# Performance work log

Measured on AMD Instinct MI355X. Metric: run time of the kernel, lower is better.

The kernel has to match this reference:

```python
import jax, jax.numpy as jnp
import numpy as np

NEG_INF = float('-inf')


def setup_inputs() -> dict:
    key = jax.random.key(0)
    ks = jax.random.split(key, 5)
    Sq, Sk, H, D, B = 4096, 4096, 8, 128, 4
    q = jax.random.normal(ks[0], (Sq, H, D), jnp.float32)
    k_local = jax.random.normal(ks[1], (Sk, H, D), jnp.float32)
    v_local = jax.random.normal(ks[2], (Sk, H, D), jnp.float32)
    k_remote = jax.random.normal(ks[3], (Sk, H, D), jnp.float32)
    v_remote = jax.random.normal(ks[4], (Sk, H, D), jnp.float32)
    # 4 ragged range pairs: equal blocks of 1024 q-tokens <-> 1024 kv-tokens
    blk = Sq // B
    starts = jnp.arange(B, dtype=jnp.int32) * blk
    ranges = jnp.stack([starts, starts + blk], axis=1)  # [B, 2]
    return dict(
        q=q, k_local=k_local, v_local=v_local,
        k_remote=k_remote, v_remote=v_remote,
        q_ranges_local=ranges, kv_ranges_local=ranges,
        is_causal_local=jnp.ones((B,), bool),
        q_ranges_remote=ranges, kv_ranges_remote=ranges,
        is_causal_remote=jnp.zeros((B,), bool),
    )


def _range_mask(Sq, Sk, q_ranges, kv_ranges, is_causal):
    # Build [Sq, Sk] attend-mask from ragged (q,kv) range pairs.
    qpos = jnp.arange(Sq)[None, :, None]   # [1, Sq, 1]
    kpos = jnp.arange(Sk)[None, None, :]   # [1, 1, Sk]
    qs = q_ranges[:, 0][:, None, None]; qe = q_ranges[:, 1][:, None, None]
    ks = kv_ranges[:, 0][:, None, None]; ke = kv_ranges[:, 1][:, None, None]
    in_q = (qpos >= qs) & (qpos < qe)
    in_k = (kpos >= ks) & (kpos < ke)
    # bottom-right-aligned causal within each range pair
    shift = (ke - ks) - (qe - qs)
    caus = (kpos - ks) <= (qpos - qs) + shift
    m = in_q & in_k & (caus | ~is_causal[:, None, None])  # [B, Sq, Sk]
    return jnp.any(m, axis=0)  # [Sq, Sk]


def _flex_attn(q, k, v, q_ranges, kv_ranges, is_causal):
    # q: [Sq, H, D]; k, v: [Sk, H, D] -> out [Sq, H, D], lse [H, Sq]
    Sq, H, D = q.shape
    Sk = k.shape[0]
    mask = _range_mask(Sq, Sk, q_ranges, kv_ranges, is_causal)  # [Sq, Sk]
    scale = 1.0 / np.sqrt(D).astype(np.float32)
    scores = jnp.einsum('qhd,khd->hqk', q, k) * scale
    scores = jnp.where(mask[None], scores, NEG_INF)
    mx = jnp.max(scores, axis=-1)                      # [H, Sq]
    mx_safe = jnp.where(jnp.isneginf(mx), 0.0, mx)
    e = jnp.where(mask[None], jnp.exp(scores - mx_safe[..., None]), 0.0)
    s = jnp.sum(e, axis=-1)                            # [H, Sq]
    lse = jnp.where(s > 0, mx_safe + jnp.log(jnp.where(s > 0, s, 1.0)), NEG_INF)
    p = e / jnp.where(s > 0, s, 1.0)[..., None]
    out = jnp.einsum('hqk,khd->qhd', p, v)
    return out, lse


def _safe_subtract(a, b):
    both_ninf = (a == b) & jnp.isneginf(a)
    return jnp.where(both_ninf, NEG_INF, a - b)


def _correct_lse(lse1, lse2):
    mn = jnp.minimum(lse1, lse2).astype(jnp.float32)
    mx = jnp.maximum(lse1, lse2).astype(jnp.float32)
    return (mx + jax.nn.softplus(_safe_subtract(mn, mx))).astype(lse1.dtype)


def _correct_out(o1, lse1, o2, lse2, lse):
    # lse*: [H, Sq] -> weights [Sq, H, 1]
    w1 = jnp.exp(_safe_subtract(lse1, lse)).T[..., None].astype(jnp.float32)
    w2 = jnp.exp(_safe_subtract(lse2, lse)).T[..., None].astype(jnp.float32)
    return (w1 * o1 + w2 * o2).astype(o1.dtype)


def _result_correction(out_list, lse_list, overlap_degree):
    # Faithful to the original loop structure (stage 1 merged twice).
    curr_lse = _correct_lse(lse_list[0], lse_list[1])
    curr_out = _correct_out(out_list[0], lse_list[0], out_list[1], lse_list[1], curr_lse)
    for i in range(overlap_degree):
        orig_lse, orig_out = curr_lse, curr_out
        curr_lse = _correct_lse(orig_lse, lse_list[i + 1])
        curr_out = _correct_out(orig_out, orig_lse, out_list[i + 1], lse_list[i + 1], curr_lse)
    return curr_out, curr_lse


def reference(q, k_local, v_local, k_remote, v_remote,
              q_ranges_local, kv_ranges_local, is_causal_local,
              q_ranges_remote, kv_ranges_remote, is_causal_remote):
    o0, l0 = _flex_attn(q, k_local, v_local, q_ranges_local, kv_ranges_local, is_causal_local)
    o1, l1 = _flex_attn(q, k_remote, v_remote, q_ranges_remote, kv_ranges_remote, is_causal_remote)
    out, lse = _result_correction([o0, o1], [l0, l1], overlap_degree=1)
    return out, lse
```

## Files before the change

kernel.cpp:

```cpp
#include <hip/hip_runtime.h>
#include <math.h>
#include <limits.h>


constexpr int NH = 8;
constexpr int DH = 128;
#define NEG_INF (-INFINITY)

typedef __bf16 bf16x8 __attribute__((ext_vector_type(8)));
typedef float  f32x4  __attribute__((ext_vector_type(4)));
typedef float  f32x16 __attribute__((ext_vector_type(16)));

__device__ __forceinline__ unsigned short f2bf_rne(float x) {
  union { float f; unsigned u; } v; v.f = x;
  unsigned r = v.u + 0x7FFFu + ((v.u >> 16) & 1u);
  return (unsigned short)(r >> 16);
}
__device__ __forceinline__ unsigned pk2(float lo, float hi) {
  return (unsigned)f2bf_rne(lo) | ((unsigned)f2bf_rne(hi) << 16);
}
__device__ __forceinline__ unsigned cvtpk_bf16(float lo, float hi) {
  unsigned r;
  asm("v_cvt_pk_bf16_f32 %0, %1, %2" : "=v"(r) : "v"(lo), "v"(hi));
  return r;
}
__device__ __forceinline__ void gl2lds16(const void* g, void* l) {
  __builtin_amdgcn_global_load_lds(
      (const __attribute__((address_space(1))) unsigned int*)g,
      (__attribute__((address_space(3))) unsigned int*)l, 16, 0, 0);
}
#define MFMA32 __builtin_amdgcn_mfma_f32_32x32x16_bf16

__global__ void prep_kernel(const float* __restrict__ kl, const float* __restrict__ kr,
                            const float* __restrict__ vl, const float* __restrict__ vr,
                            unsigned short* __restrict__ Kb,
                            unsigned short* __restrict__ Vt, int Sk) {
  __shared__ unsigned short T[64 * 132];
  const int nk = Sk >> 2;
  const int npan = Sk >> 6;
  const int t = threadIdx.x;
  int bid = blockIdx.x;

  if (bid < 2 * nk) {
    const int src = bid >= nk;
    const int x = src ? bid - nk : bid;
    const float* in = src ? kr : kl;
    unsigned short* o = Kb + (size_t)src * NH * Sk * DH;
    const size_t base = (size_t)x * 4096;
    #pragma unroll
    for (int rdx = 0; rdx < 4; ++rdx) {
      const size_t L = base + rdx * 1024 + (size_t)t * 4;
      float4 f = *(const float4*)(in + L);
      const int kv  = (int)(L >> 10);
      const int rem = (int)(L & 1023);
      const int h = rem >> 7, d = rem & 127;
      const int pe = (((d >> 3) ^ (kv & 7)) << 3) + (d & 7);
      uint2 w = make_uint2(pk2(f.x, f.y), pk2(f.z, f.w));
      *(uint2*)&o[((size_t)h * Sk + kv) * DH + pe] = w;
    }
  } else {
    bid -= 2 * nk;
    const int nv = npan * NH;
    const int src = bid >= nv;
    if (src) bid -= nv;
    const int h = bid / npan;
    const int x = bid % npan;
    const float* in = src ? vr : vl;
    const int kv0 = x * 64;
    unsigned short* panel =
        Vt + (((size_t)src * NH + h) * npan + x) * (DH * 64);
    {
      const int off = (t & 31) * 4;
      const int kvr_ = t >> 5;
      #pragma unroll
      for (int rdx = 0; rdx < 8; ++rdx) {
        const int kv = rdx * 8 + kvr_;
        float4 f = *(const float4*)(in + ((size_t)(kv0 + kv) * NH + h) * DH + off);
        *(uint2*)&T[kv * 132 + off] = make_uint2(pk2(f.x, f.y), pk2(f.z, f.w));
      }
    }
    __syncthreads();
    #pragma unroll
    for (int rdx = 0; rdx < 4; ++rdx) {
      const int G = rdx * 256 + t;
      const int d = G >> 3, gphys = G & 7;
      const int gk = gphys ^ (d & 7);
      unsigned short v[8];
      #pragma unroll
      for (int j = 0; j < 8; ++j) v[j] = T[(gk * 8 + j) * 132 + d];
      *(uint4*)&panel[(size_t)G * 8] = *(uint4*)v;
    }
  }
}

struct TS { int src, b, kv0, qs, qe, ks, ke, causal, shift, kendb; };

__global__ __launch_bounds__(256, 2)
void fa_kernel(const float* __restrict__ qp,
               const unsigned short* __restrict__ Kb,
               const unsigned short* __restrict__ Vt,
               const int* __restrict__ qrl, const int* __restrict__ kvrl,
               const int* __restrict__ czl,
               const int* __restrict__ qrr, const int* __restrict__ kvrr,
               const int* __restrict__ czr,
               float* __restrict__ outp, float* __restrict__ lsep,
               unsigned short* __restrict__ pO, float* __restrict__ pL,
               int Sq, int Sk, int B, int nsplit, int direct)
{
  __shared__ __align__(16) unsigned short Klds[2][64 * DH];
  __shared__ __align__(16) unsigned short Vlds[2][DH * 64];
  __shared__ float Lsc[4][32];

  const int tid = threadIdx.x, wave = tid >> 6, lane = tid & 63;
  const int dl = lane & 31, hi = lane >> 5;
  const int bid = blockIdx.x;
  const int h   = bid & 7;
  const int nqt = Sq >> 7;
  const int tt  = bid >> 3;
  int qtile = tt % nqt;
  const int split = tt / nqt;
  if (split & 1) qtile = nqt - 1 - qtile;
  const int q0 = qtile * 128;
  const int qw = q0 + wave * 32;
  const int qg = qw + dl;

  const float kscale = 0.12751743f;

  bf16x8 qfB[8];
  {
    const float* gq = qp + ((size_t)qg * NH + h) * DH + hi * 8;
    #pragma unroll
    for (int dc = 0; dc < 8; ++dc) {
      float4 a = *(const float4*)(gq + dc * 16);
      float4 b = *(const float4*)(gq + dc * 16 + 4);
      uint4 t = { pk2(a.x,a.y), pk2(a.z,a.w), pk2(b.x,b.y), pk2(b.z,b.w) };
      qfB[dc] = __builtin_bit_cast(bf16x8, t);
    }
  }

  f32x16 accO[4];
  #pragma unroll
  for (int i = 0; i < 4; ++i) accO[i] = (f32x16)(0.0f);
  float lacc = 0.0f;

  auto nextTile = [&](TS& t) -> bool {
    t.kv0 += nsplit * 64;
    while (t.kv0 >= t.kendb) {
      ++t.b;
      if (t.b >= B) {
        t.b = -1; ++t.src;
        if (t.src >= 2) return false;
        t.kendb = INT_MIN; t.kv0 = 0;
        continue;
      }
      const int* qr  = t.src ? qrr : qrl;
      const int* kvr = t.src ? kvrr : kvrl;
      const int* cz  = t.src ? czr : czl;
      t.qs = qr[2*t.b]; t.qe = qr[2*t.b+1];
      t.ks = kvr[2*t.b]; t.ke = kvr[2*t.b+1];
      if (t.qe <= q0 || t.qs >= q0 + 128 || t.ks >= t.ke) {
        t.kendb = INT_MIN; t.kv0 = 0; continue;
      }
      t.causal = cz[t.b] != 0;
      t.shift = (t.ke - t.ks) - (t.qe - t.qs);
      const int qmaxb = min(q0 + 127, t.qe - 1);
      t.kendb = t.causal ? min(t.ke, t.ks + (qmaxb - t.qs) + t.shift + 1) : t.ke;
      t.kv0 = ((t.ks >> 6) << 6) + split * 64;
    }
    return true;
  };

  auto stageTile = [&](const TS& t, int bi) {
    const unsigned short* kbh = Kb + ((size_t)t.src * NH + h) * (size_t)Sk * DH;
    const char* gk = (const char*)(kbh + (size_t)t.kv0 * DH) + wave * 4096 + lane * 16;
    char* lk = (char*)&Klds[bi][0] + wave * 4096 + lane * 16;
    #pragma unroll
    for (int i = 0; i < 4; ++i) gl2lds16(gk + i * 1024, lk + i * 1024);
    const unsigned short* vth = Vt + ((size_t)t.src * NH + h) * ((size_t)(Sk >> 6) * DH * 64);
    const char* gv = (const char*)(vth + (size_t)(t.kv0 >> 6) * (DH * 64)) + wave * 4096 + lane * 16;
    char* lv = (char*)&Vlds[bi][0] + wave * 4096 + lane * 16;
    #pragma unroll
    for (int i = 0; i < 4; ++i) gl2lds16(gv + i * 1024, lv + i * 1024);
  };

  TS cur; cur.src = 0; cur.b = -1; cur.kv0 = 0; cur.kendb = INT_MIN;
  cur.qs = 0; cur.qe = 0; cur.ks = 0; cur.ke = 0; cur.causal = 0; cur.shift = 0;
  bool haveCur = nextTile(cur);
  if (haveCur) stageTile(cur, 0);
  __syncthreads();
  int buf = 0;

  while (haveCur) {
    TS nxt = cur;
    const bool haveNxt = nextTile(nxt);
    if (haveNxt) stageTile(nxt, buf ^ 1);

    int wkend = INT_MIN;
    {
      const int wqs = max(qw, cur.qs), wqe = min(qw + 32, cur.qe);
      if (wqs < wqe) {
        const int wqmax = min(qw + 31, cur.qe - 1);
        wkend = cur.causal
              ? min(cur.ke, cur.ks + (wqmax - cur.qs) + cur.shift + 1)
              : cur.ke;
      }
    }

    if (cur.kv0 < wkend) {
      const int kv0 = cur.kv0, ks = cur.ks, ke = cur.ke;
      const int qs = cur.qs, qe = cur.qe, causal = cur.causal, shift = cur.shift;
      const float sbias = cur.src ? 1.0f : 0.0f;

      f32x16 S0 = (f32x16)(0.0f), S1 = (f32x16)(0.0f);
      const unsigned short* kb = &Klds[buf][0];
      __builtin_amdgcn_s_setprio(1);
      #pragma unroll
      for (int dc = 0; dc < 8; ++dc) {
        const int ph = ((dc * 2 + hi) ^ (dl & 7)) << 3;
        bf16x8 k0 = *(const bf16x8*)&kb[dl * DH + ph];
        bf16x8 k1 = *(const bf16x8*)&kb[(32 + dl) * DH + ph];
        S0 = MFMA32(k0, qfB[dc], S0, 0, 0, 0);
        S1 = MFMA32(k1, qfB[dc], S1, 0, 0, 0);
      }
      __builtin_amdgcn_s_setprio(0);

      const bool interior = (kv0 >= ks) && (kv0 + 64 <= ke) &&
                            (qw >= qs) && (qw + 32 <= qe) &&
                            (!causal || (kv0 + 63 - ks) <= (qw - qs) + shift);
      if (!interior) {
        const int qok = (qg >= qs) && (qg < qe);
        const int lo = ks - kv0;
        int up = ke - kv0 - 1;
        if (causal) up = min(up, (qg - qs) + shift + (ks - kv0));
        #pragma unroll
        for (int r = 0; r < 16; ++r) {
          const int kt = (r & 3) + 8 * (r >> 2) + 4 * hi;
          const int ok0 = qok && (kt >= lo) && (kt <= up);
          const int ok1 = qok && (kt + 32 >= lo) && (kt + 32 <= up);
          S0[r] = ok0 ? S0[r] : NEG_INF;
          S1[r] = ok1 ? S1[r] : NEG_INF;
        }
      }

      float p0[16], p1[16];
      #pragma unroll
      for (int r = 0; r < 16; ++r) {
        p0[r] = __builtin_amdgcn_exp2f(S0[r] * kscale + sbias);
        p1[r] = __builtin_amdgcn_exp2f(S1[r] * kscale + sbias);
      }
      {
        float t0 = 0.f, t1 = 0.f, t2 = 0.f, t3 = 0.f;
        #pragma unroll
        for (int r = 0; r < 4; ++r) {
          t0 += p0[r];      t1 += p0[r + 4];
          t2 += p0[r + 8];  t3 += p0[r + 12];
          t0 += p1[r];      t1 += p1[r + 4];
          t2 += p1[r + 8];  t3 += p1[r + 12];
        }
        lacc += (t0 + t1) + (t2 + t3);
      }

      __builtin_amdgcn_s_setprio(1);
      #define PVKC(pp, kc)                                                        \
      {                                                                           \
        const unsigned a0 = cvtpk_bf16(pp[((kc)&1)*8+0], pp[((kc)&1)*8+1]);       \
        const unsigned a1 = cvtpk_bf16(pp[((kc)&1)*8+2], pp[((kc)&1)*8+3]);       \
        const unsigned b0 = cvtpk_bf16(pp[((kc)&1)*8+4], pp[((kc)&1)*8+5]);       \
        const unsigned b1 = cvtpk_bf16(pp[((kc)&1)*8+6], pp[((kc)&1)*8+7]);       \
        auto s0 = __builtin_amdgcn_permlane32_swap((int)a0, (int)b0, false, false);\
        auto s1 = __builtin_amdgcn_permlane32_swap((int)a1, (int)b1, false, false);\
        uint4 pw = { (unsigned)s0[0], (unsigned)s1[0],                            \
                     (unsigned)s0[1], (unsigned)s1[1] };                          \
        const bf16x8 pa = __builtin_bit_cast(bf16x8, pw);                         \
        const int ph = (((kc) * 2 + hi) ^ (dl & 7)) << 3;                         \
        _Pragma("unroll")                                                         \
        for (int dt = 0; dt < 4; ++dt) {                                          \
          bf16x8 vf = *(const bf16x8*)&Vlds[buf][(dt * 32 + dl) * 64 + ph];       \
          accO[dt] = MFMA32(pa, vf, accO[dt], 0, 0, 0);                           \
        }                                                                         \
      }
      PVKC(p0, 0) PVKC(p0, 1) PVKC(p1, 2) PVKC(p1, 3)
      #undef PVKC
      __builtin_amdgcn_s_setprio(0);
    }

    __syncthreads();
    cur = nxt; haveCur = haveNxt; buf ^= 1;
  }

  const float tot = lacc + __shfl_xor(lacc, 32);
  if (lane < 32) Lsc[wave][lane] = tot;
  __syncthreads();

  if (direct) {
    if (lane < 32)
      lsep[(size_t)h * Sq + qg] =
          tot > 0.f ? 0.6931471805599453f * __builtin_amdgcn_logf(tot) : NEG_INF;
    #pragma unroll
    for (int r = 0; r < 16; ++r) {
      const int qrow = (r & 3) + 8 * (r >> 2) + 4 * hi;
      const float sum = Lsc[wave][qrow];
      const float rcp = sum > 0.f ? 1.0f / sum : 0.0f;
      float* op = outp + ((size_t)(qw + qrow) * NH + h) * DH + dl;
      #pragma unroll
      for (int dt = 0; dt < 4; ++dt)
        op[dt * 32] = accO[dt][r] * rcp;
    }
  } else {
    if (lane < 32) pL[((size_t)split * NH + h) * Sq + qg] = tot;
    #pragma unroll
    for (int r = 0; r < 16; ++r) {
      const int qrow = (r & 3) + 8 * (r >> 2) + 4 * hi;
      unsigned short* pr = pO + (((size_t)split * Sq + (qw + qrow)) * NH + h) * DH + dl;
      #pragma unroll
      for (int dt = 0; dt < 4; ++dt)
        pr[dt * 32] = f2bf_rne(accO[dt][r]);
    }
  }
}

__global__ void merge_kernel(const unsigned short* __restrict__ pO,
                             const float* __restrict__ pL,
                             float* __restrict__ outp, float* __restrict__ lsep,
                             int Sq, int nsplit) {
  const int t = threadIdx.x;
  const int row = blockIdx.x * 4 + (t >> 6);
  const int dp = t & 63;
  const int q = row >> 3, h = row & 7;
  float s = 0.f, o0 = 0.f, o1 = 0.f;
  for (int sp = 0; sp < nsplit; ++sp) {
    s += pL[((size_t)sp * NH + h) * Sq + q];
    unsigned u = *(const unsigned*)&pO[(((size_t)sp * Sq + q) * NH + h) * DH + dp * 2];
    o0 += __builtin_bit_cast(float, u << 16);
    o1 += __builtin_bit_cast(float, u & 0xffff0000u);
  }
  const float rcp = s > 0.f ? 1.0f / s : 0.f;
  *(float2*)&outp[(size_t)row * DH + dp * 2] = make_float2(o0 * rcp, o1 * rcp);
  if (dp == 0)
    lsep[(size_t)h * Sq + q] =
        s > 0.f ? 0.6931471805599453f * __builtin_amdgcn_logf(s) : NEG_INF;
}

extern "C" void kernel_launch(void* const* d_in, const int* in_sizes, int n_in,
                              void* d_out, int out_size, void* d_ws, size_t ws_size,
                              hipStream_t stream) {
  const float* qp = (const float*)d_in[0];
  const float* kl = (const float*)d_in[1];
  const float* vl = (const float*)d_in[2];
  const float* kr = (const float*)d_in[3];
  const float* vr = (const float*)d_in[4];
  const int* qrl  = (const int*)d_in[5];
  const int* kvrl = (const int*)d_in[6];
  const int* czl  = (const int*)d_in[7];
  const int* qrr  = (const int*)d_in[8];
  const int* kvrr = (const int*)d_in[9];
  const int* czr  = (const int*)d_in[10];

  const int B  = in_sizes[5] / 2;
  const int Sq = in_sizes[0] / (NH * DH);
  const int Sk = in_sizes[1] / (NH * DH);
  float* outp = (float*)d_out;
  float* lsep = outp + (size_t)Sq * NH * DH;

  const size_t TEN  = (size_t)NH * Sk * DH;
  const size_t base = 4 * TEN * sizeof(unsigned short);
  unsigned short* Kb = (unsigned short*)d_ws;
  unsigned short* Vt = Kb + 2 * TEN;

  auto needO = [&](int ns) {
    return (size_t)ns * Sq * NH * DH * 2 + (size_t)ns * NH * Sq * 4;
  };
  int ns; int direct = 0;
  if      (ws_size >= base + needO(2)) ns = 2;
  else if (ws_size >= base + needO(1)) ns = 1;
  else { ns = 1; direct = 1; }
  unsigned short* pO = (unsigned short*)((char*)d_ws + base);
  float* pL = (float*)((char*)d_ws + base + (size_t)ns * Sq * NH * DH * 2);

  const int prep_blocks = 2 * (Sk / 4) + 2 * (Sk / 64) * NH;
  prep_kernel<<<dim3(prep_blocks), 256, 0, stream>>>(kl, kr, vl, vr, Kb, Vt, Sk);

  fa_kernel<<<dim3(ns * (Sq / 128) * NH), 256, 0, stream>>>(
      qp, Kb, Vt, qrl, kvrl, czl, qrr, kvrr, czr,
      outp, lsep, pO, pL, Sq, Sk, B, ns, direct);

  if (!direct)
    merge_kernel<<<dim3(Sq * NH / 4), 256, 0, stream>>>(pO, pL, outp, lsep, Sq, ns);
}
```

Measured before the change: 178.2 us.

## Rework K/V LDS swizzles, fold softmax scale into Q, unroll double-buffer loop

Widens the K swizzle from 8 to 16 chunks and changes the V panel layout so two d-rows share each 128-element row with an XOR swizzle, aiming to cut LDS bank conflicts. The softmax scale moves into the Q bf16 conversion and the remote-source factor of two moves into V preprocessing and the row-sum accumulation, which removes a per-element FMA before exp2. The main loop is manually unrolled by two so buffer indices are compile-time constants. Pre-scaling Q before the bf16 rounding changes rounding behaviour slightly, and the unbalanced-tile shortcut in the unrolled loop needs care to stay correct.

Measured after the change: 177.2 us. About the same (-0.6%).

```diff
diff --git a/kernel.cpp b/kernel.cpp
--- a/kernel.cpp
+++ b/kernel.cpp
@@ -54,7 +54,7 @@
       const int kv  = (int)(L >> 10);
       const int rem = (int)(L & 1023);
       const int h = rem >> 7, d = rem & 127;
-      const int pe = (((d >> 3) ^ (kv & 7)) << 3) + (d & 7);
+      const int pe = (((d >> 3) ^ (kv & 15)) << 3) + (d & 7);
       uint2 w = make_uint2(pk2(f.x, f.y), pk2(f.z, f.w));
       *(uint2*)&o[((size_t)h * Sk + kv) * DH + pe] = w;
     }
@@ -66,6 +66,7 @@
     const int h = bid / npan;
     const int x = bid % npan;
     const float* in = src ? vr : vl;
+    const float vscl = src ? 2.0f : 1.0f;
     const int kv0 = x * 64;
     unsigned short* panel =
         Vt + (((size_t)src * NH + h) * npan + x) * (DH * 64);
@@ -76,18 +77,21 @@
       for (int rdx = 0; rdx < 8; ++rdx) {
         const int kv = rdx * 8 + kvr_;
         float4 f = *(const float4*)(in + ((size_t)(kv0 + kv) * NH + h) * DH + off);
-        *(uint2*)&T[kv * 132 + off] = make_uint2(pk2(f.x, f.y), pk2(f.z, f.w));
+        *(uint2*)&T[kv * 132 + off] =
+            make_uint2(pk2(f.x * vscl, f.y * vscl), pk2(f.z * vscl, f.w * vscl));
       }
     }
     __syncthreads();
     #pragma unroll
     for (int rdx = 0; rdx < 4; ++rdx) {
       const int G = rdx * 256 + t;
-      const int d = G >> 3, gphys = G & 7;
-      const int gk = gphys ^ (d & 7);
+      const int r = G >> 4, sp = G & 15;
+      const int s = sp ^ ((r & 7) << 1);
+      const int d = 2 * r + (s & 1);
+      const int g = s >> 1;
       unsigned short v[8];
       #pragma unroll
-      for (int j = 0; j < 8; ++j) v[j] = T[(gk * 8 + j) * 132 + d];
+      for (int j = 0; j < 8; ++j) v[j] = T[(g * 8 + j) * 132 + d];
       *(uint4*)&panel[(size_t)G * 8] = *(uint4*)v;
     }
   }
@@ -108,7 +112,7 @@
                int Sq, int Sk, int B, int nsplit, int direct)
 {
   __shared__ __align__(16) unsigned short Klds[2][64 * DH];
-  __shared__ __align__(16) unsigned short Vlds[2][DH * 64];
+  __shared__ __align__(16) unsigned short Vlds[2][64 * DH];
   __shared__ float Lsc[4][32];
 
   const int tid = threadIdx.x, wave = tid >> 6, lane = tid & 63;
@@ -133,7 +137,8 @@
     for (int dc = 0; dc < 8; ++dc) {
       float4 a = *(const float4*)(gq + dc * 16);
       float4 b = *(const float4*)(gq + dc * 16 + 4);
-      uint4 t = { pk2(a.x,a.y), pk2(a.z,a.w), pk2(b.x,b.y), pk2(b.z,b.w) };
+      uint4 t = { pk2(a.x * kscale, a.y * kscale), pk2(a.z * kscale, a.w * kscale),
+                  pk2(b.x * kscale, b.y * kscale), pk2(b.z * kscale, b.w * kscale) };
       qfB[dc] = __builtin_bit_cast(bf16x8, t);
     }
   }
@@ -170,122 +175,130 @@
     return true;
   };
 
-  auto stageTile = [&](const TS& t, int bi) {
+  auto stageTile = [&](const TS& t, unsigned short* lkb, unsigned short* lvb) {
     const unsigned short* kbh = Kb + ((size_t)t.src * NH + h) * (size_t)Sk * DH;
     const char* gk = (const char*)(kbh + (size_t)t.kv0 * DH) + wave * 4096 + lane * 16;
-    char* lk = (char*)&Klds[bi][0] + wave * 4096 + lane * 16;
+    char* lk = (char*)lkb + wave * 4096 + lane * 16;
     #pragma unroll
     for (int i = 0; i < 4; ++i) gl2lds16(gk + i * 1024, lk + i * 1024);
     const unsigned short* vth = Vt + ((size_t)t.src * NH + h) * ((size_t)(Sk >> 6) * DH * 64);
     const char* gv = (const char*)(vth + (size_t)(t.kv0 >> 6) * (DH * 64)) + wave * 4096 + lane * 16;
-    char* lv = (char*)&Vlds[bi][0] + wave * 4096 + lane * 16;
+    char* lv = (char*)lvb + wave * 4096 + lane * 16;
     #pragma unroll
     for (int i = 0; i < 4; ++i) gl2lds16(gv + i * 1024, lv + i * 1024);
   };
 
+  auto computeTile = [&](const TS& t, const unsigned short* kb,
+                         const unsigned short* vb) {
+    int wkend = INT_MIN;
+    {
+      const int wqs = max(qw, t.qs), wqe = min(qw + 32, t.qe);
+      if (wqs < wqe) {
+        const int wqmax = min(qw + 31, t.qe - 1);
+        wkend = t.causal
+              ? min(t.ke, t.ks + (wqmax - t.qs) + t.shift + 1)
+              : t.ke;
+      }
+    }
+    if (t.kv0 >= wkend) return;
+    const int kv0 = t.kv0, ks = t.ks, ke = t.ke;
+    const int qs = t.qs, qe = t.qe, causal = t.causal, shift = t.shift;
+
+    f32x16 S0 = (f32x16)(0.0f), S1 = (f32x16)(0.0f);
+    __builtin_amdgcn_s_setprio(1);
+    #pragma unroll
+    for (int dc = 0; dc < 8; ++dc) {
+      const int ph = ((dc * 2 + hi) ^ (dl & 15)) << 3;
+      bf16x8 k0 = *(const bf16x8*)&kb[dl * DH + ph];
+      bf16x8 k1 = *(const bf16x8*)&kb[(32 + dl) * DH + ph];
+      S0 = MFMA32(k0, qfB[dc], S0, 0, 0, 0);
+      S1 = MFMA32(k1, qfB[dc], S1, 0, 0, 0);
+    }
+    __builtin_amdgcn_s_setprio(0);
+
+    const bool interior = (kv0 >= ks) && (kv0 + 64 <= ke) &&
+                          (qw >= qs) && (qw + 32 <= qe) &&
+                          (!causal || (kv0 + 63 - ks) <= (qw - qs) + shift);
+    if (!interior) {
+      const int qok = (qg >= qs) && (qg < qe);
+      const int lo = ks - kv0;
+      int up = ke - kv0 - 1;
+      if (causal) up = min(up, (qg - qs) + shift + (ks - kv0));
+      #pragma unroll
+      for (int r = 0; r < 16; ++r) {
+        const int kt = (r & 3) + 8 * (r >> 2) + 4 * hi;
+        const int ok0 = qok && (kt >= lo) && (kt <= up);
+        const int ok1 = qok && (kt + 32 >= lo) && (kt + 32 <= up);
+        S0[r] = ok0 ? S0[r] : NEG_INF;
+        S1[r] = ok1 ? S1[r] : NEG_INF;
+      }
+    }
+
+    float p0[16], p1[16];
+    #pragma unroll
+    for (int r = 0; r < 16; ++r) {
+      p0[r] = __builtin_amdgcn_exp2f(S0[r]);
+      p1[r] = __builtin_amdgcn_exp2f(S1[r]);
+    }
+    {
+      float t0 = 0.f, t1 = 0.f, t2 = 0.f, t3 = 0.f;
+      #pragma unroll
+      for (int r = 0; r < 4; ++r) {
+        t0 += p0[r];      t1 += p0[r + 4];
+        t2 += p0[r + 8];  t3 += p0[r + 12];
+        t0 += p1[r];      t1 += p1[r + 4];
+        t2 += p1[r + 8];  t3 += p1[r + 12];
+      }
+      const float ts = (t0 + t1) + (t2 + t3);
+      lacc += t.src ? 2.0f * ts : ts;
+    }
+
+    __builtin_amdgcn_s_setprio(1);
+    const int vrow = (dl >> 1) * 128;
+    #define PVKC(pp, kc)                                                        \
+    {                                                                           \
+      const unsigned a0 = cvtpk_bf16(pp[((kc)&1)*8+0], pp[((kc)&1)*8+1]);       \
+      const unsigned a1 = cvtpk_bf16(pp[((kc)&1)*8+2], pp[((kc)&1)*8+3]);       \
+      const unsigned b0 = cvtpk_bf16(pp[((kc)&1)*8+4], pp[((kc)&1)*8+5]);       \
+      const unsigned b1 = cvtpk_bf16(pp[((kc)&1)*8+6], pp[((kc)&1)*8+7]);       \
+      auto s0 = __builtin_amdgcn_permlane32_swap((int)a0, (int)b0, false, false);\
+      auto s1 = __builtin_amdgcn_permlane32_swap((int)a1, (int)b1, false, false);\
+      uint4 pw = { (unsigned)s0[0], (unsigned)s1[0],                            \
+                   (unsigned)s0[1], (unsigned)s1[1] };                          \
+      const bf16x8 pa = __builtin_bit_cast(bf16x8, pw);                         \
+      const int sp = ((((kc)*2+hi) << 1) | (dl & 1)) ^ (((dl >> 1) & 7) << 1);  \
+      const int vbase = vrow + sp * 8;                                          \
+      _Pragma("unroll")                                                         \
+      for (int dt = 0; dt < 4; ++dt) {                                          \
+        bf16x8 vf = *(const bf16x8*)&vb[dt * 2048 + vbase];                     \
+        accO[dt] = MFMA32(pa, vf, accO[dt], 0, 0, 0);                           \
+      }                                                                         \
+    }
+    PVKC(p0, 0) PVKC(p0, 1) PVKC(p1, 2) PVKC(p1, 3)
+    #undef PVKC
+    __builtin_amdgcn_s_setprio(0);
+  };
+
   TS cur; cur.src = 0; cur.b = -1; cur.kv0 = 0; cur.kendb = INT_MIN;
   cur.qs = 0; cur.qe = 0; cur.ks = 0; cur.ke = 0; cur.causal = 0; cur.shift = 0;
-  bool haveCur = nextTile(cur);
-  if (haveCur) stageTile(cur, 0);
+  bool hc = nextTile(cur);
+  TS nx = cur;
+  bool hn = hc ? nextTile(nx) : false;
+  if (hc) stageTile(cur, &Klds[0][0], &Vlds[0][0]);
   __syncthreads();
-  int buf = 0;
-
-  while (haveCur) {
-    TS nxt = cur;
-    const bool haveNxt = nextTile(nxt);
-    if (haveNxt) stageTile(nxt, buf ^ 1);
-
-    int wkend = INT_MIN;
-    {
-      const int wqs = max(qw, cur.qs), wqe = min(qw + 32, cur.qe);
-      if (wqs < wqe) {
-        const int wqmax = min(qw + 31, cur.qe - 1);
-        wkend = cur.causal
-              ? min(cur.ke, cur.ks + (wqmax - cur.qs) + cur.shift + 1)
-              : cur.ke;
-      }
-    }
-
-    if (cur.kv0 < wkend) {
-      const int kv0 = cur.kv0, ks = cur.ks, ke = cur.ke;
-      const int qs = cur.qs, qe = cur.qe, causal = cur.causal, shift = cur.shift;
-      const float sbias = cur.src ? 1.0f : 0.0f;
-
-      f32x16 S0 = (f32x16)(0.0f), S1 = (f32x16)(0.0f);
-      const unsigned short* kb = &Klds[buf][0];
-      __builtin_amdgcn_s_setprio(1);
-      #pragma unroll
-      for (int dc = 0; dc < 8; ++dc) {
-        const int ph = ((dc * 2 + hi) ^ (dl & 7)) << 3;
-        bf16x8 k0 = *(const bf16x8*)&kb[dl * DH + ph];
-        bf16x8 k1 = *(const bf16x8*)&kb[(32 + dl) * DH + ph];
-        S0 = MFMA32(k0, qfB[dc], S0, 0, 0, 0);
-        S1 = MFMA32(k1, qfB[dc], S1, 0, 0, 0);
-      }
-      __builtin_amdgcn_s_setprio(0);
-
-      const bool interior = (kv0 >= ks) && (kv0 + 64 <= ke) &&
-                            (qw >= qs) && (qw + 32 <= qe) &&
-                            (!causal || (kv0 + 63 - ks) <= (qw - qs) + shift);
-      if (!interior) {
-        const int qok = (qg >= qs) && (qg < qe);
-        const int lo = ks - kv0;
-        int up = ke - kv0 - 1;
-        if (causal) up = min(up, (qg - qs) + shift + (ks - kv0));
-        #pragma unroll
-        for (int r = 0; r < 16; ++r) {
-          const int kt = (r & 3) + 8 * (r >> 2) + 4 * hi;
-          const int ok0 = qok && (kt >= lo) && (kt <= up);
-          const int ok1 = qok && (kt + 32 >= lo) && (kt + 32 <= up);
-          S0[r] = ok0 ? S0[r] : NEG_INF;
-          S1[r] = ok1 ? S1[r] : NEG_INF;
-        }
-      }
-
-      float p0[16], p1[16];
-      #pragma unroll
-      for (int r = 0; r < 16; ++r) {
-        p0[r] = __builtin_amdgcn_exp2f(S0[r] * kscale + sbias);
-        p1[r] = __builtin_amdgcn_exp2f(S1[r] * kscale + sbias);
-      }
-      {
-        float t0 = 0.f, t1 = 0.f, t2 = 0.f, t3 = 0.f;
-        #pragma unroll
-        for (int r = 0; r < 4; ++r) {
-          t0 += p0[r];      t1 += p0[r + 4];
-          t2 += p0[r + 8];  t3 += p0[r + 12];
-          t0 += p1[r];      t1 += p1[r + 4];
-          t2 += p1[r + 8];  t3 += p1[r + 12];
-        }
-        lacc += (t0 + t1) + (t2 + t3);
-      }
-
-      __builtin_amdgcn_s_setprio(1);
-      #define PVKC(pp, kc)                                                        \
-      {                                                                           \
-        const unsigned a0 = cvtpk_bf16(pp[((kc)&1)*8+0], pp[((kc)&1)*8+1]);       \
-        const unsigned a1 = cvtpk_bf16(pp[((kc)&1)*8+2], pp[((kc)&1)*8+3]);       \
-        const unsigned b0 = cvtpk_bf16(pp[((kc)&1)*8+4], pp[((kc)&1)*8+5]);       \
-        const unsigned b1 = cvtpk_bf16(pp[((kc)&1)*8+6], pp[((kc)&1)*8+7]);       \
-        auto s0 = __builtin_amdgcn_permlane32_swap((int)a0, (int)b0, false, false);\
-        auto s1 = __builtin_amdgcn_permlane32_swap((int)a1, (int)b1, false, false);\
-        uint4 pw = { (unsigned)s0[0], (unsigned)s1[0],                            \
-                     (unsigned)s0[1], (unsigned)s1[1] };                          \
-        const bf16x8 pa = __builtin_bit_cast(bf16x8, pw);                         \
-        const int ph = (((kc) * 2 + hi) ^ (dl & 7)) << 3;                         \
-        _Pragma("unroll")                                                         \
-        for (int dt = 0; dt < 4; ++dt) {                                          \
-          bf16x8 vf = *(const bf16x8*)&Vlds[buf][(dt * 32 + dl) * 64 + ph];       \
-          accO[dt] = MFMA32(pa, vf, accO[dt], 0, 0, 0);                           \
-        }                                                                         \
-      }
-      PVKC(p0, 0) PVKC(p0, 1) PVKC(p1, 2) PVKC(p1, 3)
-      #undef PVKC
-      __builtin_amdgcn_s_setprio(0);
-    }
-
+
+  while (hc) {
+    if (hn) stageTile(nx, &Klds[1][0], &Vlds[1][0]);
+    computeTile(cur, &Klds[0][0], &Vlds[0][0]);
     __syncthreads();
-    cur = nxt; haveCur = haveNxt; buf ^= 1;
+    cur = nx; hc = hn;
+    if (hc) hn = nextTile(nx);
+    if (!hc) break;
+    if (hn) stageTile(nx, &Klds[0][0], &Vlds[0][0]);
+    computeTile(cur, &Klds[1][0], &Vlds[1][0]);
+    __syncthreads();
+    cur = nx; hc = hn;
+    if (hc) hn = nextTile(nx);
   }
 
   const float tot = lacc + __shfl_xor(lacc, 32);
```
